# Kernel tuning notes

Hardware: AMD Instinct MI355X
Metric: run time of the kernel (lower is better)

The kernel has to match this reference:

```python
import jax, jax.numpy as jnp
import numpy as np

DIM = 512
N_DAYS = 24

def setup_inputs() -> dict:
    key = jax.random.key(0)
    k1, k2, k3, k4 = jax.random.split(key, 4)
    x = jax.random.normal(k1, (64, 1024, DIM), dtype=jnp.float32)
    day_ids = jax.random.randint(k2, (64,), 0, N_DAYS, dtype=jnp.int64)
    W = jax.random.normal(k3, (N_DAYS, DIM, DIM), dtype=jnp.float32) * 0.02 + jnp.eye(DIM, dtype=jnp.float32)
    b = jax.random.normal(k4, (N_DAYS, DIM), dtype=jnp.float32) * 0.02
    return {"x": x, "day_ids": day_ids, "W": W, "b": b}

def reference(x, day_ids, W, b):
    # Gather per-sample day weights/biases, batched matmul + bias, softsign.
    # (Dropout is identity in eval mode.)
    Wd = W[day_ids]            # [B, dim, dim]
    bd = b[day_ids][:, None, :]  # [B, 1, dim]
    y = jnp.einsum('btd,bde->bte', x, Wd) + bd
    return y / (1.0 + jnp.abs(y))  # Softsign
```

## Files before the change

### kernel.cpp

```cpp
#include <hip/hip_runtime.h>


#define DIM 512
#define SEQ 1024
#define BM 128
#define BN 128
#define BK 32
#define LDK 40

typedef __bf16 bf16x8 __attribute__((ext_vector_type(8)));
typedef __bf16 bf16x4 __attribute__((ext_vector_type(4)));
typedef float  f32x4  __attribute__((ext_vector_type(4)));

__global__ __launch_bounds__(256, 2)
void day_adapter_kernel(const float* __restrict__ x,
                        const int*   __restrict__ day_ids,
                        const float* __restrict__ W,
                        const float* __restrict__ bias,
                        float*       __restrict__ out)
{
    __shared__ __align__(16) __bf16 As[BM][LDK];
    __shared__ __align__(16) __bf16 Bs[BN][LDK];

    const int tid = threadIdx.x;
    const int bb  = blockIdx.z;
    const int m0  = blockIdx.y * BM;
    const int n0  = blockIdx.x * BN;
    const int day = day_ids[bb];

    const float* xb = x   + (size_t)bb  * SEQ * DIM + (size_t)m0 * DIM;
    const float* Wb = W   + (size_t)day * DIM * DIM + n0;
    float*       ob = out + (size_t)bb  * SEQ * DIM + (size_t)m0 * DIM + n0;

    const int a_row = tid >> 3;
    const int a_col = (tid & 7) * 4;
    const int b_k = tid & 31;
    const int b_n = (tid >> 5) * 16;

    const int wave = tid >> 6;
    const int lane = tid & 63;
    const int wm   = (wave >> 1) * 64;
    const int wn   = (wave & 1) * 64;
    const int l15  = lane & 15;
    const int kq   = (lane >> 4) * 8;

    f32x4 acc[4][4];
    const f32x4 zero = {0.f, 0.f, 0.f, 0.f};
    #pragma unroll
    for (int i = 0; i < 4; ++i)
        #pragma unroll
        for (int j = 0; j < 4; ++j)
            acc[i][j] = zero;

    for (int kk = 0; kk < DIM; kk += BK) {
        #pragma unroll
        for (int t = 0; t < 4; ++t) {
            const int r = a_row + t * 32;
            const float4 f = *(const float4*)(xb + (size_t)r * DIM + kk + a_col);
            bf16x4 v;
            v[0] = (__bf16)f.x; v[1] = (__bf16)f.y;
            v[2] = (__bf16)f.z; v[3] = (__bf16)f.w;
            *(bf16x4*)&As[r][a_col] = v;
        }
        {
            const float* src = Wb + (size_t)(kk + b_k) * DIM + b_n;
            const float4 g0 = ((const float4*)src)[0];
            const float4 g1 = ((const float4*)src)[1];
            const float4 g2 = ((const float4*)src)[2];
            const float4 g3 = ((const float4*)src)[3];
            const float v[16] = {g0.x,g0.y,g0.z,g0.w, g1.x,g1.y,g1.z,g1.w,
                                 g2.x,g2.y,g2.z,g2.w, g3.x,g3.y,g3.z,g3.w};
            #pragma unroll
            for (int i = 0; i < 16; ++i)
                Bs[b_n + i][b_k] = (__bf16)v[i];
        }
        __syncthreads();

        bf16x8 af[4], bfr[4];
        #pragma unroll
        for (int t = 0; t < 4; ++t)
            af[t] = *(const bf16x8*)&As[wm + t * 16 + l15][kq];
        #pragma unroll
        for (int t = 0; t < 4; ++t)
            bfr[t] = *(const bf16x8*)&Bs[wn + t * 16 + l15][kq];

        #pragma unroll
        for (int i = 0; i < 4; ++i)
            #pragma unroll
            for (int j = 0; j < 4; ++j)
                acc[i][j] = __builtin_amdgcn_mfma_f32_16x16x32_bf16(
                    af[i], bfr[j], acc[i][j], 0, 0, 0);

        __syncthreads();
    }

    float bv[4];
    #pragma unroll
    for (int j = 0; j < 4; ++j)
        bv[j] = bias[(size_t)day * DIM + n0 + wn + j * 16 + l15];

    #pragma unroll
    for (int i = 0; i < 4; ++i) {
        const int rbase = wm + i * 16 + (lane >> 4) * 4;
        #pragma unroll
        for (int j = 0; j < 4; ++j) {
            const int col = wn + j * 16 + l15;
            #pragma unroll
            for (int r = 0; r < 4; ++r) {
                const float y = acc[i][j][r] + bv[j];
                ob[(size_t)(rbase + r) * DIM + col] = y / (1.0f + fabsf(y));
            }
        }
    }
}

extern "C" void kernel_launch(void* const* d_in, const int* in_sizes, int n_in,
                              void* d_out, int out_size, void* d_ws, size_t ws_size,
                              hipStream_t stream) {
    const float* x        = (const float*)d_in[0];
    const int*   day_ids  = (const int*)  d_in[1];
    const float* W        = (const float*)d_in[2];
    const float* bias     = (const float*)d_in[3];
    float*       out      = (float*)d_out;

    dim3 grid(DIM / BN, SEQ / BM, 64);
    day_adapter_kernel<<<grid, 256, 0, stream>>>(x, day_ids, W, bias, out);
}
```

Measured before the change: 317.4 us.

## Pre-transpose W to bf16 workspace and load B tiles via direct-to-LDS loads

Adds a pre-pass kernel that converts all 24 day weight matrices to bf16 in transposed (n-major) layout in the workspace. The main GEMM then loads B tiles with global_load_lds 16-byte transfers into an XOR-swizzled LDS layout, which removes the per-element fp32-to-bf16 convert and the scattered transposed LDS stores. It also doubles BK to 64, raises occupancy hints to 4 blocks per CU, and remaps the 1D grid so blocks sharing x rows run adjacently. The trade-off is an extra transpose launch over all days, including unused ones, plus higher LDS per block.

New measurement: 279.2 us. -12.0%, faster.

```diff
diff --git a/kernel.cpp b/kernel.cpp
--- a/kernel.cpp
+++ b/kernel.cpp
@@ -3,94 +3,137 @@
 
 #define DIM 512
 #define SEQ 1024
+#define NB 64
+#define NDAYS 24
 #define BM 128
 #define BN 128
-#define BK 32
-#define LDK 40
+#define BK 64
+#define LDA (BK + 8)
 
 typedef __bf16 bf16x8 __attribute__((ext_vector_type(8)));
 typedef __bf16 bf16x4 __attribute__((ext_vector_type(4)));
 typedef float  f32x4  __attribute__((ext_vector_type(4)));
 
-__global__ __launch_bounds__(256, 2)
+__device__ __forceinline__ void gll16(const void* g, void* l) {
+    __builtin_amdgcn_global_load_lds(
+        (const __attribute__((address_space(1))) unsigned int*)g,
+        (__attribute__((address_space(3))) unsigned int*)l,
+        16, 0, 0);
+}
+
+__global__ __launch_bounds__(256)
+void transpose_w_kernel(const float* __restrict__ W, __bf16* __restrict__ Wt) {
+    __shared__ __bf16 T[32][33];
+    const int d  = blockIdx.z;
+    const int k0 = blockIdx.x * 32;
+    const int n0 = blockIdx.y * 32;
+    const int tx = threadIdx.x & 31;
+    const int ty = threadIdx.x >> 5;
+    const float* Wd = W + (size_t)d * DIM * DIM;
+    #pragma unroll
+    for (int i = 0; i < 4; ++i) {
+        const int k = ty + i * 8;
+        T[tx][k] = (__bf16)Wd[(size_t)(k0 + k) * DIM + n0 + tx];
+    }
+    __syncthreads();
+    __bf16* Wtd = Wt + (size_t)d * DIM * DIM;
+    #pragma unroll
+    for (int i = 0; i < 4; ++i) {
+        const int n = ty + i * 8;
+        Wtd[(size_t)(n0 + n) * DIM + k0 + tx] = T[n][tx];
+    }
+}
+
+__global__ __launch_bounds__(256, 4)
 void day_adapter_kernel(const float* __restrict__ x,
                         const int*   __restrict__ day_ids,
-                        const float* __restrict__ W,
+                        const __bf16* __restrict__ Wt,
                         const float* __restrict__ bias,
                         float*       __restrict__ out)
 {
-    __shared__ __align__(16) __bf16 As[BM][LDK];
-    __shared__ __align__(16) __bf16 Bs[BN][LDK];
+    __shared__ __align__(16) __bf16 As[BM][LDA];
+    __shared__ __align__(16) __bf16 Bs[BN * BK];
 
+    const int L  = blockIdx.x;
+    const int g  = (L >> 3) & 3;
+    const int mb = (L & 7) | ((L >> 5) << 3);
+    const int m  = mb & 7;
+    const int bb = mb >> 3;
+
+    const int n0  = g * BN;
+    const int m0  = m * BM;
     const int tid = threadIdx.x;
-    const int bb  = blockIdx.z;
-    const int m0  = blockIdx.y * BM;
-    const int n0  = blockIdx.x * BN;
     const int day = day_ids[bb];
 
-    const float* xb = x   + (size_t)bb  * SEQ * DIM + (size_t)m0 * DIM;
-    const float* Wb = W   + (size_t)day * DIM * DIM + n0;
-    float*       ob = out + (size_t)bb  * SEQ * DIM + (size_t)m0 * DIM + n0;
-
-    const int a_row = tid >> 3;
-    const int a_col = (tid & 7) * 4;
-    const int b_k = tid & 31;
-    const int b_n = (tid >> 5) * 16;
+    const float*  xb  = x   + (size_t)bb  * SEQ * DIM + (size_t)m0 * DIM;
+    const __bf16* Wtb = Wt  + (size_t)day * DIM * DIM + (size_t)n0 * DIM;
+    float*        ob  = out + (size_t)bb  * SEQ * DIM + (size_t)m0 * DIM + n0;
 
     const int wave = tid >> 6;
     const int lane = tid & 63;
     const int wm   = (wave >> 1) * 64;
     const int wn   = (wave & 1) * 64;
     const int l15  = lane & 15;
-    const int kq   = (lane >> 4) * 8;
+    const int quad = lane >> 4;
+    const int kq   = quad * 8;
+
+    const int a_row = tid >> 2;
+    const int a_col = (tid & 3) * 4;
+
+    char* BsB = (char*)Bs;
 
     f32x4 acc[4][4];
     const f32x4 zero = {0.f, 0.f, 0.f, 0.f};
     #pragma unroll
     for (int i = 0; i < 4; ++i)
         #pragma unroll
-        for (int j = 0; j < 4; ++j)
-            acc[i][j] = zero;
+        for (int j = 0; j < 4; ++j) acc[i][j] = zero;
 
     for (int kk = 0; kk < DIM; kk += BK) {
         #pragma unroll
-        for (int t = 0; t < 4; ++t) {
-            const int r = a_row + t * 32;
-            const float4 f = *(const float4*)(xb + (size_t)r * DIM + kk + a_col);
-            bf16x4 v;
-            v[0] = (__bf16)f.x; v[1] = (__bf16)f.y;
-            v[2] = (__bf16)f.z; v[3] = (__bf16)f.w;
-            *(bf16x4*)&As[r][a_col] = v;
+        for (int p = 0; p < 4; ++p) {
+            const int s  = p * 256 + tid;
+            const int n  = s >> 3;
+            const int cp = s & 7;
+            const int c  = cp ^ (n & 7);
+            gll16(Wtb + (size_t)n * DIM + kk + c * 8,
+                  BsB + (size_t)(p * 256 + (tid & ~63)) * 16);
         }
-        {
-            const float* src = Wb + (size_t)(kk + b_k) * DIM + b_n;
-            const float4 g0 = ((const float4*)src)[0];
-            const float4 g1 = ((const float4*)src)[1];
-            const float4 g2 = ((const float4*)src)[2];
-            const float4 g3 = ((const float4*)src)[3];
-            const float v[16] = {g0.x,g0.y,g0.z,g0.w, g1.x,g1.y,g1.z,g1.w,
-                                 g2.x,g2.y,g2.z,g2.w, g3.x,g3.y,g3.z,g3.w};
+        #pragma unroll
+        for (int h = 0; h < 2; ++h) {
+            const int r = a_row + h * 64;
             #pragma unroll
-            for (int i = 0; i < 16; ++i)
-                Bs[b_n + i][b_k] = (__bf16)v[i];
+            for (int i = 0; i < 4; ++i) {
+                const int col = a_col + i * 16;
+                const float4 f = *(const float4*)(xb + (size_t)r * DIM + kk + col);
+                bf16x4 v;
+                v[0] = (__bf16)f.x; v[1] = (__bf16)f.y;
+                v[2] = (__bf16)f.z; v[3] = (__bf16)f.w;
+                *(bf16x4*)&As[r][col] = v;
+            }
         }
         __syncthreads();
 
-        bf16x8 af[4], bfr[4];
         #pragma unroll
-        for (int t = 0; t < 4; ++t)
-            af[t] = *(const bf16x8*)&As[wm + t * 16 + l15][kq];
-        #pragma unroll
-        for (int t = 0; t < 4; ++t)
-            bfr[t] = *(const bf16x8*)&Bs[wn + t * 16 + l15][kq];
-
-        #pragma unroll
-        for (int i = 0; i < 4; ++i)
+        for (int ks = 0; ks < 2; ++ks) {
+            bf16x8 af[4], bfr[4];
             #pragma unroll
-            for (int j = 0; j < 4; ++j)
-                acc[i][j] = __builtin_amdgcn_mfma_f32_16x16x32_bf16(
-                    af[i], bfr[j], acc[i][j], 0, 0, 0);
-
+            for (int i = 0; i < 4; ++i)
+                af[i] = *(const bf16x8*)&As[wm + i * 16 + l15][ks * 32 + kq];
+            #pragma unroll
+            for (int j = 0; j < 4; ++j) {
+                const int n  = wn + j * 16 + l15;
+                const int c  = ks * 4 + quad;
+                const int cp = c ^ (n & 7);
+                bfr[j] = *(const bf16x8*)&Bs[n * BK + cp * 8];
+            }
+            #pragma unroll
+            for (int i = 0; i < 4; ++i)
+                #pragma unroll
+                for (int j = 0; j < 4; ++j)
+                    acc[i][j] = __builtin_amdgcn_mfma_f32_16x16x32_bf16(
+                        af[i], bfr[j], acc[i][j], 0, 0, 0);
+        }
         __syncthreads();
     }
 
@@ -101,7 +144,7 @@
 
     #pragma unroll
     for (int i = 0; i < 4; ++i) {
-        const int rbase = wm + i * 16 + (lane >> 4) * 4;
+        const int rbase = wm + i * 16 + quad * 4;
         #pragma unroll
         for (int j = 0; j < 4; ++j) {
             const int col = wn + j * 16 + l15;
@@ -117,12 +160,15 @@
 extern "C" void kernel_launch(void* const* d_in, const int* in_sizes, int n_in,
                               void* d_out, int out_size, void* d_ws, size_t ws_size,
                               hipStream_t stream) {
-    const float* x        = (const float*)d_in[0];
-    const int*   day_ids  = (const int*)  d_in[1];
-    const float* W        = (const float*)d_in[2];
-    const float* bias     = (const float*)d_in[3];
-    float*       out      = (float*)d_out;
+    const float* x       = (const float*)d_in[0];
+    const int*   day_ids = (const int*)  d_in[1];
+    const float* W       = (const float*)d_in[2];
+    const float* bias    = (const float*)d_in[3];
+    float*       out     = (float*)d_out;
+    __bf16*      Wt      = (__bf16*)d_ws;
 
-    dim3 grid(DIM / BN, SEQ / BM, 64);
-    day_adapter_kernel<<<grid, 256, 0, stream>>>(x, day_ids, W, bias, out);
+    dim3 tgrid(DIM / 32, DIM / 32, NDAYS);
+    transpose_w_kernel<<<tgrid, 256, 0, stream>>>(W, Wt);
+
+    day_adapter_kernel<<<dim3(2048), 256, 0, stream>>>(x, day_ids, Wt, bias, out);
 }
```
